# Kernel tuning notes

Measured on AMD Instinct MI355X. Metric: run time of the kernel, lower is better.

Reference implementation:

```python
import jax, jax.numpy as jnp
import numpy as np

N_HEAD = 16

def setup_inputs() -> dict:
    key = jax.random.key(0)
    ks = jax.random.split(key, 7)
    B, T, C = 2, 2048, 1024
    return {
        "query": jax.random.normal(ks[0], (B, T, C), jnp.float32),
        "key": jax.random.normal(ks[1], (B, T, C), jnp.float32),
        "value": jax.random.normal(ks[2], (B, T, C), jnp.float32),
        "Wq": jax.random.normal(ks[3], (C, C), jnp.float32) * (1.0 / np.sqrt(C)),
        "Wk": jax.random.normal(ks[4], (C, C), jnp.float32) * (1.0 / np.sqrt(C)),
        "Wv": jax.random.normal(ks[5], (C, C), jnp.float32) * (1.0 / np.sqrt(C)),
        "Wo": jax.random.normal(ks[6], (C, C), jnp.float32) * (1.0 / np.sqrt(C)),
    }

def reference(query, key, value, Wq, Wk, Wv, Wo):
    B, T, C = query.shape
    H = N_HEAD
    D = C // H
    # QKV projections (torch Linear: x @ W.T, no bias)
    q = (query @ Wq.T).reshape(B, T, H, D).transpose(0, 2, 1, 3)  # [B,H,T,D]
    k = (key   @ Wk.T).reshape(B, T, H, D).transpose(0, 2, 1, 3)
    v = (value @ Wv.T).reshape(B, T, H, D).transpose(0, 2, 1, 3)
    scale = 1.0 / np.sqrt(D).astype(np.float32)
    att = jnp.einsum("bhqd,bhkd->bhqk", q, k) * scale  # [B,H,T,T]
    att = jax.nn.softmax(att, axis=-1)
    y = jnp.einsum("bhqk,bhkd->bhqd", att, v)  # [B,H,T,D]
    y = y.transpose(0, 2, 1, 3).reshape(B, T, C)
    return y @ Wo.T
```

## Files before the change

### kernel.cpp

```cpp
#include <hip/hip_runtime.h>
#include <hip/hip_bf16.h>
#include <cstdint>

typedef __attribute__((ext_vector_type(8))) short bf16x8;
typedef __attribute__((ext_vector_type(4))) float f32x4;
typedef __attribute__((ext_vector_type(16))) float f32x16;
typedef __attribute__((ext_vector_type(4))) unsigned short us4;

#define MFMA16(a, b, c) __builtin_amdgcn_mfma_f32_16x16x32_bf16((a), (b), (c), 0, 0, 0)
#define MFMA32(a, b, c) __builtin_amdgcn_mfma_f32_32x32x16_bf16((a), (b), (c), 0, 0, 0)
#define GLB_PTR(p) ((const __attribute__((address_space(1))) void*)(p))
#define LDS_PTR(p) ((__attribute__((address_space(3))) void*)(p))

__device__ __forceinline__ unsigned short f2bf(float f) {
    union { float f; unsigned u; } v; v.f = f;
    unsigned r = v.u + 0x7fffu + ((v.u >> 16) & 1u);
    return (unsigned short)(r >> 16);
}

__device__ __forceinline__ unsigned cvtpk(float lo, float hi) {
    unsigned r;
    asm("v_cvt_pk_bf16_f32 %0, %1, %2" : "=v"(r) : "v"(lo), "v"(hi));
    return r;
}

struct CastArgs {
    const float* src[7];
    unsigned short* dst[7];
    int n4[7];
};

__global__ __launch_bounds__(256) void cast_f32_bf16(CastArgs a) {
    const int id = blockIdx.y;
    const float4* s = (const float4*)a.src[id];
    us4* d = (us4*)a.dst[id];
    const int n4 = a.n4[id];
    for (int i = blockIdx.x * blockDim.x + threadIdx.x; i < n4;
         i += gridDim.x * blockDim.x) {
        float4 v = s[i];
        us4 o;
        o.x = f2bf(v.x); o.y = f2bf(v.y); o.z = f2bf(v.z); o.w = f2bf(v.w);
        d[i] = o;
    }
}

struct GemmGroup {
    const unsigned short* A[3];
    const unsigned short* B[3];
    unsigned short* C[3];
};

__global__ __launch_bounds__(256, 2)
void gemm_qkv(GemmGroup gg, int M, int N, int K) {
    __shared__ __align__(16) unsigned short As[128 * 32];
    __shared__ __align__(16) unsigned short Bs[128 * 32];
    const int z = blockIdx.z;
    const unsigned short* __restrict__ A = gg.A[z];
    const unsigned short* __restrict__ B = gg.B[z];
    unsigned short* __restrict__ C = gg.C[z];
    const int t = threadIdx.x;
    const int lane = t & 63, wave = t >> 6;
    const int row0 = blockIdx.x * 128, col0 = blockIdx.y * 128;
    const int wr = (wave >> 1) * 64, wc = (wave & 1) * 64;
    const int r = lane & 15, g = lane >> 4;
    const int srow = t >> 2;
    const int scol = (t & 3) * 8;

    f32x4 acc[4][4] = {};

    for (int k0 = 0; k0 < K; k0 += 32) {
#pragma unroll
        for (int i = 0; i < 2; ++i) {
            const int rr = i * 64 + srow;
            __builtin_amdgcn_global_load_lds(
                GLB_PTR(A + (size_t)(row0 + rr) * K + k0 + scol),
                LDS_PTR(As + rr * 32 + scol), 16, 0, 0);
            __builtin_amdgcn_global_load_lds(
                GLB_PTR(B + (size_t)(col0 + rr) * K + k0 + scol),
                LDS_PTR(Bs + rr * 32 + scol), 16, 0, 0);
        }
        __syncthreads();
        bf16x8 a[4], b[4];
#pragma unroll
        for (int m = 0; m < 4; ++m)
            a[m] = *(const bf16x8*)(As + (wr + m * 16 + r) * 32 + g * 8);
#pragma unroll
        for (int n = 0; n < 4; ++n)
            b[n] = *(const bf16x8*)(Bs + (wc + n * 16 + r) * 32 + g * 8);
#pragma unroll
        for (int m = 0; m < 4; ++m)
#pragma unroll
            for (int n = 0; n < 4; ++n)
                acc[m][n] = MFMA16(a[m], b[n], acc[m][n]);
        __syncthreads();
    }

    const float sc = (z == 0) ? 0.18033688011112042f : 1.0f;
#pragma unroll
    for (int m = 0; m < 4; ++m) {
#pragma unroll
        for (int n = 0; n < 4; ++n) {
#pragma unroll
            for (int i = 0; i < 4; ++i) {
                const int row = row0 + wr + m * 16 + g * 4 + i;
                const int col = col0 + wc + n * 16 + r;
                const int b_ = row >> 11, tt = row & 2047;
                const int h = col >> 6, d = col & 63;
                const int bh = b_ * 16 + h;
                size_t idx;
                if (z == 2) {
                    const int l = (d & 31) + 32 * ((tt >> 3) & 1);
                    idx = ((((size_t)(bh * 32 + (tt >> 6))) * 2 + (d >> 5)) * 4 +
                           ((tt >> 4) & 3)) * 512 + l * 8 + (tt & 7);
                } else {
                    const int l = (tt & 31) + 32 * ((d >> 3) & 1);
                    idx = (((size_t)(bh * 64 + (tt >> 5))) * 4 + (d >> 4)) * 512 +
                          l * 8 + (d & 7);
                }
                C[idx] = f2bf(acc[m][n][i] * sc);
            }
        }
    }
}

template <int TM>
__global__ __launch_bounds__(256, 2)
void gemm_wo(const unsigned short* __restrict__ A,
             const unsigned short* __restrict__ B,
             float* __restrict__ C, int M, int N, int K) {
    constexpr int MN = (TM == 128) ? 4 : 2;
    __shared__ __align__(16) unsigned short As[TM * 32];
    __shared__ __align__(16) unsigned short Bs[128 * 32];
    const int t = threadIdx.x;
    const int lane = t & 63, wave = t >> 6;
    const int row0 = blockIdx.x * TM, col0 = blockIdx.y * 128;
    const int wr = (TM == 128) ? (wave >> 1) * 64 : 0;
    const int wc = (TM == 128) ? (wave & 1) * 64 : wave * 32;
    const int r = lane & 15, g = lane >> 4;
    const int srow = t >> 2;
    const int scol = (t & 3) * 8;

    f32x4 acc[4][MN] = {};

    for (int k0 = 0; k0 < K; k0 += 32) {
#pragma unroll
        for (int i = 0; i < TM / 64; ++i) {
            const int rr = i * 64 + srow;
            __builtin_amdgcn_global_load_lds(
                GLB_PTR(A + (size_t)(row0 + rr) * K + k0 + scol),
                LDS_PTR(As + rr * 32 + scol), 16, 0, 0);
        }
#pragma unroll
        for (int i = 0; i < 2; ++i) {
            const int rr = i * 64 + srow;
            __builtin_amdgcn_global_load_lds(
                GLB_PTR(B + (size_t)(col0 + rr) * K + k0 + scol),
                LDS_PTR(Bs + rr * 32 + scol), 16, 0, 0);
        }
        __syncthreads();
        bf16x8 a[4], b[MN];
#pragma unroll
        for (int m = 0; m < 4; ++m)
            a[m] = *(const bf16x8*)(As + (wr + m * 16 + r) * 32 + g * 8);
#pragma unroll
        for (int n = 0; n < MN; ++n)
            b[n] = *(const bf16x8*)(Bs + (wc + n * 16 + r) * 32 + g * 8);
#pragma unroll
        for (int m = 0; m < 4; ++m)
#pragma unroll
            for (int n = 0; n < MN; ++n)
                acc[m][n] = MFMA16(a[m], b[n], acc[m][n]);
        __syncthreads();
    }

#pragma unroll
    for (int m = 0; m < 4; ++m)
#pragma unroll
        for (int n = 0; n < MN; ++n)
#pragma unroll
            for (int i = 0; i < 4; ++i) {
                const int row = row0 + wr + m * 16 + g * 4 + i;
                const int col = col0 + wc + n * 16 + r;
                C[(size_t)row * N + col] = acc[m][n][i];
            }
}

__global__ __launch_bounds__(256, 2)
void attn_fwd(const unsigned short* __restrict__ Qpk,
              const unsigned short* __restrict__ Kpk,
              const unsigned short* __restrict__ Vpk,
              unsigned short* __restrict__ Y) {
    __shared__ __align__(16) unsigned short kv_lds[2][16][512];
    const int t = threadIdx.x, lane = t & 63, w = t >> 6;
    const int q31 = lane & 31, hi = lane >> 5;

    const int flat = blockIdx.x + 16 * blockIdx.y;
    const int swz = (flat & 7) * 64 + (flat >> 3);
    const int qt = swz & 15, bh = swz >> 4;
    const int qb0 = qt * 128;

    const unsigned short* Qb = Qpk + ((size_t)(bh * 64 + qt * 4 + w)) * 2048;
    const unsigned short* Kb = Kpk + (size_t)bh * 131072;
    const unsigned short* Vb = Vpk + (size_t)bh * 131072;

    bf16x8 qf[4];
#pragma unroll
    for (int s = 0; s < 4; ++s)
        qf[s] = *(const bf16x8*)(Qb + s * 512 + lane * 8);

    f32x16 o0 = {}, o1 = {};
    float l_ = 0.f;

#define STAGE(buf, kv0)                                                        \
    {                                                                          \
        _Pragma("unroll")                                                      \
        for (int i = 0; i < 4; ++i) {                                          \
            const int f = w * 4 + i;                                           \
            const unsigned short* src =                                        \
                (f < 8 ? Kb : Vb) + (kv0) * 64 + (f & 7) * 512 + lane * 8;     \
            __builtin_amdgcn_global_load_lds(                                  \
                GLB_PTR(src), LDS_PTR(&kv_lds[buf][f][lane * 8]), 16, 0, 0);   \
        }                                                                      \
    }

    STAGE(0, 0);
    __syncthreads();

    for (int it = 0; it < 32; ++it) {
        const int buf = it & 1;
        if (it + 1 < 32) STAGE(buf ^ 1, (it + 1) * 64);

        bf16x8 kf[8];
#pragma unroll
        for (int i = 0; i < 8; ++i)
            kf[i] = *(const bf16x8*)(&kv_lds[buf][i][lane * 8]);
        f32x16 s0, s1;
#pragma unroll
        for (int r = 0; r < 16; ++r) { s0[r] = -12.f; s1[r] = -12.f; }
        __builtin_amdgcn_s_setprio(1);
#pragma unroll
        for (int s = 0; s < 4; ++s) s0 = MFMA32(kf[s], qf[s], s0);
#pragma unroll
        for (int s = 0; s < 4; ++s) s1 = MFMA32(kf[4 + s], qf[s], s1);
        __builtin_amdgcn_s_setprio(0);

        float p[32];
#pragma unroll
        for (int r = 0; r < 16; ++r) p[r] = __builtin_amdgcn_exp2f(s0[r]);
#pragma unroll
        for (int r = 0; r < 16; ++r) p[16 + r] = __builtin_amdgcn_exp2f(s1[r]);

        float sm[16];
#pragma unroll
        for (int r = 0; r < 16; ++r) sm[r] = p[r] + p[16 + r];
#pragma unroll
        for (int d = 8; d > 0; d >>= 1)
#pragma unroll
            for (int r = 0; r < d; ++r) sm[r] += sm[r + d];
        l_ += sm[0] + __shfl_xor(sm[0], 32);

        unsigned c[16];
#pragma unroll
        for (int i = 0; i < 16; ++i) c[i] = cvtpk(p[2 * i], p[2 * i + 1]);

        bf16x8 vf[8];
#pragma unroll
        for (int i = 0; i < 8; ++i)
            vf[i] = *(const bf16x8*)(&kv_lds[buf][8 + i][lane * 8]);

        __builtin_amdgcn_s_setprio(1);
#pragma unroll
        for (int s = 0; s < 4; ++s) {
            const int base = (s >> 1) * 8 + (s & 1) * 4;
            unsigned a0 = c[base + 0], b0 = c[base + 2];
            unsigned a1 = c[base + 1], b1 = c[base + 3];
            asm volatile("v_permlane32_swap_b32 %0, %1" : "+v"(a0), "+v"(b0));
            asm volatile("v_permlane32_swap_b32 %0, %1" : "+v"(a1), "+v"(b1));
            union { unsigned u[4]; bf16x8 v; } pb;
            pb.u[0] = a0; pb.u[1] = a1; pb.u[2] = b0; pb.u[3] = b1;
            o0 = MFMA32(vf[s], pb.v, o0);
            o1 = MFMA32(vf[4 + s], pb.v, o1);
        }
        __builtin_amdgcn_s_setprio(0);

        __syncthreads();
    }
#undef STAGE

    unsigned short (*yb)[64] = (unsigned short (*)[64])kv_lds;
    const float rinv = 1.0f / l_;
#pragma unroll
    for (int r = 0; r < 16; ++r) {
        const int dd = (r & 3) + 8 * (r >> 2) + 4 * hi;
        yb[w * 32 + q31][dd] = f2bf(o0[r] * rinv);
        yb[w * 32 + q31][32 + dd] = f2bf(o1[r] * rinv);
    }
    __syncthreads();
    const int b_ = bh >> 4, h = bh & 15;
#pragma unroll
    for (int i = 0; i < 8; ++i) {
        const int row = i * 16 + (t >> 4);
        const int col = (t & 15) * 4;
        *(us4*)(Y + ((size_t)(b_ * 2048 + qb0 + row)) * 1024 + h * 64 + col) =
            *(const us4*)(&yb[row][col]);
    }
}

extern "C" void kernel_launch(void* const* d_in, const int* in_sizes, int n_in,
                              void* d_out, int out_size, void* d_ws, size_t ws_size,
                              hipStream_t stream) {
    uint8_t* ws = (uint8_t*)d_ws;
    unsigned short* xq = (unsigned short*)(ws + 0);
    unsigned short* xk = (unsigned short*)(ws + 8388608);
    unsigned short* xv = (unsigned short*)(ws + 16777216);
    unsigned short* wq = (unsigned short*)(ws + 25165824);
    unsigned short* wk = (unsigned short*)(ws + 27262976);
    unsigned short* wv = (unsigned short*)(ws + 29360128);
    unsigned short* wo = (unsigned short*)(ws + 31457280);
    unsigned short* Qp = (unsigned short*)(ws + 33554432);
    unsigned short* Kp = (unsigned short*)(ws + 41943040);
    unsigned short* Vp = (unsigned short*)(ws + 50331648);
    unsigned short* y  = xq;

    CastArgs ca;
    ca.src[0] = (const float*)d_in[0]; ca.dst[0] = xq; ca.n4[0] = 4194304 / 4;
    ca.src[1] = (const float*)d_in[1]; ca.dst[1] = xk; ca.n4[1] = 4194304 / 4;
    ca.src[2] = (const float*)d_in[2]; ca.dst[2] = xv; ca.n4[2] = 4194304 / 4;
    ca.src[3] = (const float*)d_in[3]; ca.dst[3] = wq; ca.n4[3] = 1048576 / 4;
    ca.src[4] = (const float*)d_in[4]; ca.dst[4] = wk; ca.n4[4] = 1048576 / 4;
    ca.src[5] = (const float*)d_in[5]; ca.dst[5] = wv; ca.n4[5] = 1048576 / 4;
    ca.src[6] = (const float*)d_in[6]; ca.dst[6] = wo; ca.n4[6] = 1048576 / 4;
    cast_f32_bf16<<<dim3(512, 7), 256, 0, stream>>>(ca);

    GemmGroup gg;
    gg.A[0] = xq; gg.B[0] = wq; gg.C[0] = Qp;
    gg.A[1] = xk; gg.B[1] = wk; gg.C[1] = Kp;
    gg.A[2] = xv; gg.B[2] = wv; gg.C[2] = Vp;
    gemm_qkv<<<dim3(32, 8, 3), 256, 0, stream>>>(gg, 4096, 1024, 1024);

    attn_fwd<<<dim3(16, 32), 256, 0, stream>>>(Qp, Kp, Vp, y);

    gemm_wo<64><<<dim3(64, 8), 256, 0, stream>>>(y, wo, (float*)d_out, 4096, 1024, 1024);
}
```

Measured before the change: 124.5 us.

## Double-buffer GEMM LDS stages and halve attention block size to 2 waves

Both projection GEMMs now double-buffer their LDS tiles so global loads for the next K-slice are issued before the current slice's MFMAs, and they raise wave priority around the MFMA block. The attention kernel switches from 4-wave blocks covering 128 queries to 2-wave blocks covering 64 queries. This doubles the grid to 1024 blocks to improve occupancy and load balance. The trade-off is that each K/V tile is loaded twice as often per query, and the extra LDS buffers may limit occupancy in the GEMMs. The output staging buffer is also padded to reduce LDS bank conflicts.

Result: slower. 132.7 us (+6.6%).

```diff
diff --git a/kernel.cpp b/kernel.cpp
--- a/kernel.cpp
+++ b/kernel.cpp
@@ -52,8 +52,8 @@
 
 __global__ __launch_bounds__(256, 2)
 void gemm_qkv(GemmGroup gg, int M, int N, int K) {
-    __shared__ __align__(16) unsigned short As[128 * 32];
-    __shared__ __align__(16) unsigned short Bs[128 * 32];
+    __shared__ __align__(16) unsigned short As[2][128 * 32];
+    __shared__ __align__(16) unsigned short Bs[2][128 * 32];
     const int z = blockIdx.z;
     const unsigned short* __restrict__ A = gg.A[z];
     const unsigned short* __restrict__ B = gg.B[z];
@@ -66,34 +66,44 @@
     const int srow = t >> 2;
     const int scol = (t & 3) * 8;
 
+#define GSTAGE(buf, k0)                                                        \
+    {                                                                          \
+        _Pragma("unroll")                                                      \
+        for (int i = 0; i < 2; ++i) {                                          \
+            const int rr = i * 64 + srow;                                      \
+            __builtin_amdgcn_global_load_lds(                                  \
+                GLB_PTR(A + (size_t)(row0 + rr) * K + (k0) + scol),            \
+                LDS_PTR(&As[buf][rr * 32 + scol]), 16, 0, 0);                  \
+            __builtin_amdgcn_global_load_lds(                                  \
+                GLB_PTR(B + (size_t)(col0 + rr) * K + (k0) + scol),            \
+                LDS_PTR(&Bs[buf][rr * 32 + scol]), 16, 0, 0);                  \
+        }                                                                      \
+    }
+
     f32x4 acc[4][4] = {};
-
-    for (int k0 = 0; k0 < K; k0 += 32) {
-#pragma unroll
-        for (int i = 0; i < 2; ++i) {
-            const int rr = i * 64 + srow;
-            __builtin_amdgcn_global_load_lds(
-                GLB_PTR(A + (size_t)(row0 + rr) * K + k0 + scol),
-                LDS_PTR(As + rr * 32 + scol), 16, 0, 0);
-            __builtin_amdgcn_global_load_lds(
-                GLB_PTR(B + (size_t)(col0 + rr) * K + k0 + scol),
-                LDS_PTR(Bs + rr * 32 + scol), 16, 0, 0);
-        }
-        __syncthreads();
+    GSTAGE(0, 0);
+    __syncthreads();
+
+    for (int it = 0; it < 32; ++it) {
+        const int buf = it & 1;
+        if (it + 1 < 32) GSTAGE(buf ^ 1, (it + 1) * 32);
         bf16x8 a[4], b[4];
 #pragma unroll
         for (int m = 0; m < 4; ++m)
-            a[m] = *(const bf16x8*)(As + (wr + m * 16 + r) * 32 + g * 8);
+            a[m] = *(const bf16x8*)(&As[buf][(wr + m * 16 + r) * 32 + g * 8]);
 #pragma unroll
         for (int n = 0; n < 4; ++n)
-            b[n] = *(const bf16x8*)(Bs + (wc + n * 16 + r) * 32 + g * 8);
+            b[n] = *(const bf16x8*)(&Bs[buf][(wc + n * 16 + r) * 32 + g * 8]);
+        __builtin_amdgcn_s_setprio(1);
 #pragma unroll
         for (int m = 0; m < 4; ++m)
 #pragma unroll
             for (int n = 0; n < 4; ++n)
                 acc[m][n] = MFMA16(a[m], b[n], acc[m][n]);
+        __builtin_amdgcn_s_setprio(0);
         __syncthreads();
     }
+#undef GSTAGE
 
     const float sc = (z == 0) ? 0.18033688011112042f : 1.0f;
 #pragma unroll
@@ -123,69 +133,72 @@
     }
 }
 
-template <int TM>
 __global__ __launch_bounds__(256, 2)
 void gemm_wo(const unsigned short* __restrict__ A,
              const unsigned short* __restrict__ B,
              float* __restrict__ C, int M, int N, int K) {
-    constexpr int MN = (TM == 128) ? 4 : 2;
-    __shared__ __align__(16) unsigned short As[TM * 32];
-    __shared__ __align__(16) unsigned short Bs[128 * 32];
+    __shared__ __align__(16) unsigned short As[2][64 * 32];
+    __shared__ __align__(16) unsigned short Bs[2][128 * 32];
     const int t = threadIdx.x;
     const int lane = t & 63, wave = t >> 6;
-    const int row0 = blockIdx.x * TM, col0 = blockIdx.y * 128;
-    const int wr = (TM == 128) ? (wave >> 1) * 64 : 0;
-    const int wc = (TM == 128) ? (wave & 1) * 64 : wave * 32;
+    const int row0 = blockIdx.x * 64, col0 = blockIdx.y * 128;
+    const int wc = wave * 32;
     const int r = lane & 15, g = lane >> 4;
     const int srow = t >> 2;
     const int scol = (t & 3) * 8;
 
-    f32x4 acc[4][MN] = {};
-
-    for (int k0 = 0; k0 < K; k0 += 32) {
-#pragma unroll
-        for (int i = 0; i < TM / 64; ++i) {
-            const int rr = i * 64 + srow;
-            __builtin_amdgcn_global_load_lds(
-                GLB_PTR(A + (size_t)(row0 + rr) * K + k0 + scol),
-                LDS_PTR(As + rr * 32 + scol), 16, 0, 0);
-        }
-#pragma unroll
-        for (int i = 0; i < 2; ++i) {
-            const int rr = i * 64 + srow;
-            __builtin_amdgcn_global_load_lds(
-                GLB_PTR(B + (size_t)(col0 + rr) * K + k0 + scol),
-                LDS_PTR(Bs + rr * 32 + scol), 16, 0, 0);
-        }
+#define WSTAGE(buf, k0)                                                        \
+    {                                                                          \
+        __builtin_amdgcn_global_load_lds(                                      \
+            GLB_PTR(A + (size_t)(row0 + srow) * K + (k0) + scol),              \
+            LDS_PTR(&As[buf][srow * 32 + scol]), 16, 0, 0);                    \
+        _Pragma("unroll")                                                      \
+        for (int i = 0; i < 2; ++i) {                                          \
+            const int rr = i * 64 + srow;                                      \
+            __builtin_amdgcn_global_load_lds(                                  \
+                GLB_PTR(B + (size_t)(col0 + rr) * K + (k0) + scol),            \
+                LDS_PTR(&Bs[buf][rr * 32 + scol]), 16, 0, 0);                  \
+        }                                                                      \
+    }
+
+    f32x4 acc[4][2] = {};
+    WSTAGE(0, 0);
+    __syncthreads();
+
+    for (int it = 0; it < 32; ++it) {
+        const int buf = it & 1;
+        if (it + 1 < 32) WSTAGE(buf ^ 1, (it + 1) * 32);
+        bf16x8 a[4], b[2];
+#pragma unroll
+        for (int m = 0; m < 4; ++m)
+            a[m] = *(const bf16x8*)(&As[buf][(m * 16 + r) * 32 + g * 8]);
+#pragma unroll
+        for (int n = 0; n < 2; ++n)
+            b[n] = *(const bf16x8*)(&Bs[buf][(wc + n * 16 + r) * 32 + g * 8]);
+        __builtin_amdgcn_s_setprio(1);
+#pragma unroll
+        for (int m = 0; m < 4; ++m)
+#pragma unroll
+            for (int n = 0; n < 2; ++n)
+                acc[m][n] = MFMA16(a[m], b[n], acc[m][n]);
+        __builtin_amdgcn_s_setprio(0);
         __syncthreads();
-        bf16x8 a[4], b[MN];
-#pragma unroll
-        for (int m = 0; m < 4; ++m)
-            a[m] = *(const bf16x8*)(As + (wr + m * 16 + r) * 32 + g * 8);
-#pragma unroll
-        for (int n = 0; n < MN; ++n)
-            b[n] = *(const bf16x8*)(Bs + (wc + n * 16 + r) * 32 + g * 8);
-#pragma unroll
-        for (int m = 0; m < 4; ++m)
-#pragma unroll
-            for (int n = 0; n < MN; ++n)
-                acc[m][n] = MFMA16(a[m], b[n], acc[m][n]);
-        __syncthreads();
-    }
+    }
+#undef WSTAGE
 
 #pragma unroll
     for (int m = 0; m < 4; ++m)
 #pragma unroll
-        for (int n = 0; n < MN; ++n)
+        for (int n = 0; n < 2; ++n)
 #pragma unroll
             for (int i = 0; i < 4; ++i) {
-                const int row = row0 + wr + m * 16 + g * 4 + i;
+                const int row = row0 + m * 16 + g * 4 + i;
                 const int col = col0 + wc + n * 16 + r;
                 C[(size_t)row * N + col] = acc[m][n][i];
             }
 }
 
-__global__ __launch_bounds__(256, 2)
+__global__ __launch_bounds__(128, 2)
 void attn_fwd(const unsigned short* __restrict__ Qpk,
               const unsigned short* __restrict__ Kpk,
               const unsigned short* __restrict__ Vpk,
@@ -194,12 +207,12 @@
     const int t = threadIdx.x, lane = t & 63, w = t >> 6;
     const int q31 = lane & 31, hi = lane >> 5;
 
-    const int flat = blockIdx.x + 16 * blockIdx.y;
-    const int swz = (flat & 7) * 64 + (flat >> 3);
-    const int qt = swz & 15, bh = swz >> 4;
-    const int qb0 = qt * 128;
-
-    const unsigned short* Qb = Qpk + ((size_t)(bh * 64 + qt * 4 + w)) * 2048;
+    const int flat = blockIdx.x;
+    const int swz = (flat & 7) * 128 + (flat >> 3);
+    const int qt = swz & 31, bh = swz >> 5;
+    const int qb0 = qt * 64;
+
+    const unsigned short* Qb = Qpk + ((size_t)(bh * 64 + qt * 2 + w)) * 2048;
     const unsigned short* Kb = Kpk + (size_t)bh * 131072;
     const unsigned short* Vb = Vpk + (size_t)bh * 131072;
 
@@ -214,8 +227,8 @@
 #define STAGE(buf, kv0)                                                        \
     {                                                                          \
         _Pragma("unroll")                                                      \
-        for (int i = 0; i < 4; ++i) {                                          \
-            const int f = w * 4 + i;                                           \
+        for (int i = 0; i < 8; ++i) {                                          \
+            const int f = w * 8 + i;                                           \
             const unsigned short* src =                                        \
                 (f < 8 ? Kb : Vb) + (kv0) * 64 + (f & 7) * 512 + lane * 8;     \
             __builtin_amdgcn_global_load_lds(                                  \
@@ -287,7 +300,7 @@
     }
 #undef STAGE
 
-    unsigned short (*yb)[64] = (unsigned short (*)[64])kv_lds;
+    unsigned short (*yb)[68] = (unsigned short (*)[68])kv_lds;
     const float rinv = 1.0f / l_;
 #pragma unroll
     for (int r = 0; r < 16; ++r) {
@@ -299,7 +312,7 @@
     const int b_ = bh >> 4, h = bh & 15;
 #pragma unroll
     for (int i = 0; i < 8; ++i) {
-        const int row = i * 16 + (t >> 4);
+        const int row = i * 8 + (t >> 4);
         const int col = (t & 15) * 4;
         *(us4*)(Y + ((size_t)(b_ * 2048 + qb0 + row)) * 1024 + h * 64 + col) =
             *(const us4*)(&yb[row][col]);
@@ -338,7 +351,7 @@
     gg.A[2] = xv; gg.B[2] = wv; gg.C[2] = Vp;
     gemm_qkv<<<dim3(32, 8, 3), 256, 0, stream>>>(gg, 4096, 1024, 1024);
 
-    attn_fwd<<<dim3(16, 32), 256, 0, stream>>>(Qp, Kp, Vp, y);
-
-    gemm_wo<64><<<dim3(64, 8), 256, 0, stream>>>(y, wo, (float*)d_out, 4096, 1024, 1024);
-}
+    attn_fwd<<<dim3(1024), 128, 0, stream>>>(Qp, Kp, Vp, y);
+
+    gemm_wo<<<dim3(64, 8), 256, 0, stream>>>(y, wo, (float*)d_out, 4096, 1024, 1024);
+}
```
